# Kernel optimization log

Measured on AMD Instinct MI355X. Metric: run time of the kernel, lower is better.

The kernel has to match this reference:

```python
import jax, jax.numpy as jnp
import numpy as np

B, A, D = 1024, 200, 128
H = 8
DH = D // H
TANH_CLIP = 10.0


def setup_inputs() -> dict:
    key = jax.random.key(0)
    k = jax.random.split(key, 8)
    agent_embd = jax.random.normal(k[0], (B, A, D), dtype=jnp.float32)
    # old_action must be a permutation per row (no revisits under the mask)
    old_action = jax.vmap(lambda kk: jax.random.permutation(kk, A))(
        jax.random.split(k[1], B)).astype(jnp.int32)
    s = 0.02
    W_placeholder = jax.random.uniform(k[2], (D,), jnp.float32, -1.0, 1.0)
    W_node = jax.random.normal(k[3], (D, 3 * D), jnp.float32) * s   # project_node_embeddings
    W_fixed = jax.random.normal(k[4], (D, D), jnp.float32) * s      # project_fixed_context
    W_step = jax.random.normal(k[5], (D, D), jnp.float32) * s       # project_step_context
    W_out = jax.random.normal(k[6], (D, D), jnp.float32) * s        # project_out
    return {"agent_embd": agent_embd, "old_action": old_action,
            "W_placeholder": W_placeholder, "W_node": W_node,
            "W_fixed": W_fixed, "W_step": W_step, "W_out": W_out}


def _decode(agent_embd, old_action, W_placeholder, W_node, W_fixed, W_step, W_out):
    b_, a_, d_ = agent_embd.shape
    inv_sqrt_dh = np.float32(1.0 / np.sqrt(DH))
    inv_sqrt_d = np.float32(1.0 / np.sqrt(d_))
    batch_ix = jnp.arange(b_)

    # _precompute: fixed context + per-head K/V + logit keys
    graph_embed = agent_embd.mean(axis=1)                      # [B, D]
    fixed_ctx = graph_embed @ W_fixed                          # [B, D]
    proj = agent_embd @ W_node                                 # [B, A, 3D]
    gK, gV, logit_K = jnp.split(proj, 3, axis=-1)              # each [B, A, D]
    gK = gK.reshape(b_, a_, H, DH).transpose(2, 0, 1, 3)       # [H, B, A, dh]
    gV = gV.reshape(b_, a_, H, DH).transpose(2, 0, 1, 3)       # [H, B, A, dh]

    def step(carry, xs):
        mask, prev = carry                                     # [B, A] bool, [B] int
        i, act = xs
        gathered = agent_embd[batch_ix, prev]                  # [B, D]
        step_ctx = jnp.where(i == 0, W_placeholder[None, :], gathered)
        query = fixed_ctx + step_ctx @ W_step                  # [B, D]
        mask = jnp.where(i > 0, mask.at[batch_ix, prev].set(True), mask)

        Q = query.reshape(b_, H, DH).transpose(1, 0, 2)        # [H, B, dh]
        compat = jnp.einsum('hbd,hbad->hba', Q, gK) * inv_sqrt_dh
        compat = jnp.where(mask[None, :, :], -jnp.inf, compat)  # mask_inner
        attn = jax.nn.softmax(compat, axis=-1)                 # [H, B, A]
        heads = jnp.einsum('hba,hbad->hbd', attn, gV)          # [H, B, dh]
        glimpse = heads.transpose(1, 0, 2).reshape(b_, d_) @ W_out  # [B, D]

        logits = jnp.einsum('bd,bad->ba', glimpse, logit_K) * inv_sqrt_d
        logits = jnp.tanh(logits) * TANH_CLIP
        logits = jnp.where(mask, -jnp.inf, logits)             # mask_logits
        log_p = jax.nn.log_softmax(logits, axis=-1)            # [B, A]
        lp_sel = log_p[batch_ix, act]                          # [B]
        return (mask, act), lp_sel

    mask0 = jnp.zeros((b_, a_), dtype=bool)
    prev0 = jnp.zeros((b_,), dtype=old_action.dtype)
    xs = (jnp.arange(a_), old_action.T)
    _, lps = jax.lax.scan(step, (mask0, prev0), xs)            # lps: [A, B]
    return old_action, lps.sum(axis=0)


def reference(agent_embd, old_action, W_placeholder, W_node, W_fixed, W_step, W_out):
    return _decode(agent_embd, old_action, W_placeholder, W_node, W_fixed, W_step, W_out)
```

## Files before the change

### kernel.cpp

```cpp
#include <hip/hip_runtime.h>
#include <cstdint>
#include <cstddef>

#define BB 1024
#define AA 200
#define DD 128
#define HH 8
#define N3 384

typedef unsigned short u16;
typedef unsigned int u32;
typedef __attribute__((ext_vector_type(8))) short bf16x8;
typedef __attribute__((ext_vector_type(4))) float f32x4;

__device__ __forceinline__ float bf2f(u16 v){ return __uint_as_float(((u32)v) << 16); }
__device__ __forceinline__ u16 f2bf(float f){
  u32 u = __float_as_uint(f);
  u32 r = u + 0x7fffu + ((u >> 16) & 1u);
  return (u16)(r >> 16);
}
__device__ __forceinline__ u16 f2bf_trunc(float f){
  return (u16)(__float_as_uint(f) >> 16);
}
__device__ __forceinline__ bf16x8 pack8(float4 a, float4 b){
  bf16x8 o;
  o[0] = (short)f2bf(a.x); o[1] = (short)f2bf(a.y);
  o[2] = (short)f2bf(a.z); o[3] = (short)f2bf(a.w);
  o[4] = (short)f2bf(b.x); o[5] = (short)f2bf(b.y);
  o[6] = (short)f2bf(b.z); o[7] = (short)f2bf(b.w);
  return o;
}

__global__ void k_act_rank(const int* __restrict__ oa, float* __restrict__ out0,
                           int* __restrict__ rank){
  int m = blockIdx.x * 256 + threadIdx.x;
  if (m >= BB*AA) return;
  int v = oa[m];
  out0[m] = (float)v;
  int b = m / AA;
  int j = m - b*AA;
  rank[b*AA + v] = j;
}

__global__ void k_prep(const float* __restrict__ Wn, const float* __restrict__ Ws,
                       const float* __restrict__ Wo,
                       u16* __restrict__ WnT, u16* __restrict__ WsT,
                       u16* __restrict__ WoT){
  int idx = blockIdx.x * 256 + threadIdx.x;
  if (idx < 49152){
    int n = idx >> 7, k = idx & 127;
    WnT[idx] = f2bf(Wn[k*N3 + n]);
  } else if (idx < 65536){
    int j = idx - 49152;
    int n = j >> 7, k = j & 127;
    WsT[j] = f2bf(Ws[k*DD + n]);
  } else if (idx < 81920){
    int j = idx - 65536;
    int n = j >> 7, k = j & 127;
    WoT[j] = f2bf(Wo[k*DD + n]);
  }
}

__global__ void k_fixed(const float* __restrict__ E, const float* __restrict__ Wf,
                        float* __restrict__ fixedc){
  int b = blockIdx.x;
  int d = threadIdx.x;
  __shared__ float ge[DD];
  const float* Eb = E + (size_t)b*AA*DD;
  float s = 0.f;
  for (int a = 0; a < AA; ++a) s += Eb[a*DD + d];
  ge[d] = s * (1.0f/AA);
  __syncthreads();
  float acc = 0.f;
  for (int k = 0; k < DD; ++k) acc = fmaf(ge[k], Wf[k*DD + d], acc);
  fixedc[b*DD + d] = acc;
}

__global__ __launch_bounds__(256) void k_proj_mfma(const float* __restrict__ E,
                                                   const u16* __restrict__ WnT,
                                                   u16* __restrict__ proj){
  const int t = threadIdx.x;
  const int w = t >> 6, L = t & 63;
  const int l16 = L & 15, lq = L >> 4;
  const int m0 = blockIdx.x * 128;
  const int n0 = blockIdx.y * 128;
  const int row0 = m0 + w*32;

  f32x4 acc[2][8] = {};
  const float* Arow0 = E + (size_t)(row0 + l16)*DD;
  const float* Arow1 = Arow0 + (size_t)16*DD;
  #pragma unroll
  for (int ks = 0; ks < 4; ++ks){
    int ko = ks*32 + lq*8;
    bf16x8 a0 = pack8(*(const float4*)(Arow0 + ko), *(const float4*)(Arow0 + ko + 4));
    bf16x8 a1 = pack8(*(const float4*)(Arow1 + ko), *(const float4*)(Arow1 + ko + 4));
    #pragma unroll
    for (int nt = 0; nt < 8; ++nt){
      union { uint4 u; bf16x8 v; } bb;
      bb.u = *(const uint4*)(WnT + (size_t)(n0 + nt*16 + l16)*DD + ko);
      acc[0][nt] = __builtin_amdgcn_mfma_f32_16x16x32_bf16(a0, bb.v, acc[0][nt], 0, 0, 0);
      acc[1][nt] = __builtin_amdgcn_mfma_f32_16x16x32_bf16(a1, bb.v, acc[1][nt], 0, 0, 0);
    }
  }
  #pragma unroll
  for (int mt = 0; mt < 2; ++mt)
    #pragma unroll
    for (int r = 0; r < 4; ++r){
      int row = row0 + mt*16 + lq*4 + r;
      u16* dst = proj + (size_t)row*N3 + n0;
      #pragma unroll
      for (int nt = 0; nt < 8; ++nt)
        dst[nt*16 + l16] = f2bf(acc[mt][nt][r]);
    }
}

__global__ __launch_bounds__(256) void k_query_mfma(const float* __restrict__ E,
                                                    const int* __restrict__ oa,
                                                    const float* __restrict__ Wp,
                                                    const u16* __restrict__ WsT,
                                                    const float* __restrict__ fixedc,
                                                    u16* __restrict__ qhg){
  const int t = threadIdx.x;
  const int w = t >> 6, L = t & 63;
  const int l16 = L & 15, lq = L >> 4;
  const int m0 = blockIdx.x * 128;
  const int row0 = m0 + w*32;

  const float* src[2];
  #pragma unroll
  for (int mt = 0; mt < 2; ++mt){
    int q = row0 + mt*16 + l16;
    int b = q / AA, i = q - b*AA;
    src[mt] = (i == 0) ? Wp : (E + (size_t)(b*AA + oa[b*AA + i - 1])*DD);
  }

  f32x4 acc[2][8] = {};
  #pragma unroll
  for (int ks = 0; ks < 4; ++ks){
    int ko = ks*32 + lq*8;
    bf16x8 a0 = pack8(*(const float4*)(src[0] + ko), *(const float4*)(src[0] + ko + 4));
    bf16x8 a1 = pack8(*(const float4*)(src[1] + ko), *(const float4*)(src[1] + ko + 4));
    #pragma unroll
    for (int nt = 0; nt < 8; ++nt){
      union { uint4 u; bf16x8 v; } bb;
      bb.u = *(const uint4*)(WsT + (size_t)(nt*16 + l16)*DD + ko);
      acc[0][nt] = __builtin_amdgcn_mfma_f32_16x16x32_bf16(a0, bb.v, acc[0][nt], 0, 0, 0);
      acc[1][nt] = __builtin_amdgcn_mfma_f32_16x16x32_bf16(a1, bb.v, acc[1][nt], 0, 0, 0);
    }
  }
  #pragma unroll
  for (int mt = 0; mt < 2; ++mt)
    #pragma unroll
    for (int r = 0; r < 4; ++r){
      int row = row0 + mt*16 + lq*4 + r;
      int b = row / AA;
      const float* fc = fixedc + (size_t)b*DD;
      u16* dst = qhg + (size_t)row*DD;
      #pragma unroll
      for (int nt = 0; nt < 8; ++nt)
        dst[nt*16 + l16] = f2bf((acc[mt][nt][r] + fc[nt*16 + l16]) * 0.25f);
    }
}

#define KSTR 24
#define VSTR 232
__global__ __launch_bounds__(256) void k_attn(const u16* __restrict__ proj,
                                              const int* __restrict__ rank,
                                              u16* __restrict__ qhg){
  __shared__ __align__(16) u16 KL[208*KSTR];
  __shared__ __align__(16) u16 VT[16*VSTR];
  __shared__ __align__(16) u16 P [4][16*VSTR];
  const int b = blockIdx.x;
  const int h = blockIdx.y;
  const int t = threadIdx.x;
  const int w = t >> 6, L = t & 63;
  const int l16 = L & 15, lq = L >> 4;

  for (int idx = t; idx < 208*KSTR; idx += 256) KL[idx] = 0;
  for (int idx = t; idx < 16*VSTR; idx += 256) VT[idx] = 0;
  {
    u16* Pw = P[w];
    for (int idx = L; idx < 16*VSTR; idx += 64) Pw[idx] = 0;
  }

  if (t < AA){
    const u16* src = proj + ((size_t)(b*AA + t))*N3 + h*16;
    uint4 k0 = *(const uint4*)(src);
    uint4 k1 = *(const uint4*)(src + 8);
    *(uint4*)&KL[t*KSTR]     = k0;
    *(uint4*)&KL[t*KSTR + 8] = k1;
    const u16* sv = src + 128;
    u16 d16[16];
    *(uint4*)(d16)   = *(const uint4*)(sv);
    *(uint4*)(d16+8) = *(const uint4*)(sv+8);
    #pragma unroll
    for (int d = 0; d < 16; ++d) VT[d*VSTR + t] = d16[d];
  }

  int ra[13];
  #pragma unroll
  for (int at = 0; at < 13; ++at){
    int a = at*16 + l16;
    ra[at] = (a < AA) ? rank[b*AA + a] : -1;
  }
  __syncthreads();

  u16* Qbase = qhg + (size_t)b*AA*DD + h*16;
  u16* Pw = P[w];

  const bf16x8 zf = {0,0,0,0,0,0,0,0};
  for (int it = w; it < 13; it += 4){
    bf16x8 qf = zf;
    int qi = it*16 + l16;
    if (lq < 2 && qi < AA){
      union { uint4 u; bf16x8 v; } tmp;
      tmp.u = *(const uint4*)(Qbase + (size_t)qi*DD + lq*8);
      qf = tmp.v;
    }
    f32x4 S[13];
    #pragma unroll
    for (int at = 0; at < 13; ++at){
      bf16x8 kf = zf;
      if (lq < 2){
        union { uint4 u; bf16x8 v; } tmp;
        tmp.u = *(const uint4*)&KL[(at*16 + l16)*KSTR + lq*8];
        kf = tmp.v;
      }
      f32x4 z = {0.f,0.f,0.f,0.f};
      S[at] = __builtin_amdgcn_mfma_f32_16x16x32_bf16(qf, kf, z, 0, 0, 0);
    }
    #pragma unroll
    for (int at = 0; at < 13; ++at)
      #pragma unroll
      for (int r = 0; r < 4; ++r){
        int i = it*16 + lq*4 + r;
        S[at][r] = (ra[at] < i) ? -__builtin_inff() : S[at][r];
      }
    float inv[4];
    #pragma unroll
    for (int r = 0; r < 4; ++r){
      float m = S[0][r];
      #pragma unroll
      for (int at = 1; at < 13; ++at) m = fmaxf(m, S[at][r]);
      #pragma unroll
      for (int off = 1; off < 16; off <<= 1) m = fmaxf(m, __shfl_xor(m, off));
      float sum = 0.f;
      #pragma unroll
      for (int at = 0; at < 13; ++at){
        float e = __expf(S[at][r] - m);
        S[at][r] = e; sum += e;
      }
      #pragma unroll
      for (int off = 1; off < 16; off <<= 1) sum += __shfl_xor(sum, off);
      inv[r] = 1.0f / sum;
    }
    #pragma unroll
    for (int at = 0; at < 13; ++at)
      #pragma unroll
      for (int r = 0; r < 4; ++r)
        Pw[(lq*4 + r)*VSTR + at*16 + l16] = f2bf_trunc(S[at][r]);
    f32x4 acc = {0.f,0.f,0.f,0.f};
    #pragma unroll
    for (int kb = 0; kb < 7; ++kb){
      union { uint4 u; bf16x8 v; } pa, vb;
      pa.u = *(const uint4*)&Pw[l16*VSTR + kb*32 + lq*8];
      vb.u = *(const uint4*)&VT[l16*VSTR + kb*32 + lq*8];
      acc = __builtin_amdgcn_mfma_f32_16x16x32_bf16(pa.v, vb.v, acc, 0, 0, 0);
    }
    #pragma unroll
    for (int r = 0; r < 4; ++r){
      int i = it*16 + lq*4 + r;
      if (i < AA) Qbase[(size_t)i*DD + l16] = f2bf(acc[r] * inv[r]);
    }
  }
}

__global__ __launch_bounds__(256) void k_glimpse_mfma(const u16* __restrict__ qhg,
                                                      const u16* __restrict__ WoT,
                                                      u16* __restrict__ proj){
  const int t = threadIdx.x;
  const int w = t >> 6, L = t & 63;
  const int l16 = L & 15, lq = L >> 4;
  const int m0 = blockIdx.x * 128;
  const int row0 = m0 + w*32;

  f32x4 acc[2][8] = {};
  const u16* Arow0 = qhg + (size_t)(row0 + l16)*DD;
  const u16* Arow1 = Arow0 + (size_t)16*DD;
  #pragma unroll
  for (int ks = 0; ks < 4; ++ks){
    int ko = ks*32 + lq*8;
    union { uint4 u; bf16x8 v; } a0, a1;
    a0.u = *(const uint4*)(Arow0 + ko);
    a1.u = *(const uint4*)(Arow1 + ko);
    #pragma unroll
    for (int nt = 0; nt < 8; ++nt){
      union { uint4 u; bf16x8 v; } bb;
      bb.u = *(const uint4*)(WoT + (size_t)(nt*16 + l16)*DD + ko);
      acc[0][nt] = __builtin_amdgcn_mfma_f32_16x16x32_bf16(a0.v, bb.v, acc[0][nt], 0, 0, 0);
      acc[1][nt] = __builtin_amdgcn_mfma_f32_16x16x32_bf16(a1.v, bb.v, acc[1][nt], 0, 0, 0);
    }
  }
  #pragma unroll
  for (int mt = 0; mt < 2; ++mt)
    #pragma unroll
    for (int r = 0; r < 4; ++r){
      int row = row0 + mt*16 + lq*4 + r;
      u16* dst = proj + (size_t)row*N3;
      #pragma unroll
      for (int nt = 0; nt < 8; ++nt)
        dst[nt*16 + l16] = f2bf(acc[mt][nt][r]);
    }
}

__global__ __launch_bounds__(256) void k_logits(const u16* __restrict__ proj,
                                                const int* __restrict__ rank,
                                                const int* __restrict__ oa,
                                                float* __restrict__ outlps){
  __shared__ float red[4];
  const int b = blockIdx.x;
  const int t = threadIdx.x;
  const int w = t >> 6, L = t & 63;
  const int l16 = L & 15, lq = L >> 4;
  const float inv_sqrt_d = 0.08838834764831843f;

  const u16* Gbase  = proj + (size_t)b*AA*N3;
  const u16* LKbase = Gbase + 256;

  int ra[13];
  #pragma unroll
  for (int at = 0; at < 13; ++at){
    int a = at*16 + l16;
    ra[at] = (a < AA) ? rank[b*AA + a] : -1;
  }

  float lp_part = 0.f;

  for (int it = w; it < 13; it += 4){
    bf16x8 af[4];
    {
      const u16* arow = Gbase + (size_t)(it*16 + l16)*N3;
      #pragma unroll
      for (int kb = 0; kb < 4; ++kb){
        union { uint4 u; bf16x8 v; } tmp;
        tmp.u = *(const uint4*)(arow + kb*32 + lq*8);
        af[kb] = tmp.v;
      }
    }
    f32x4 S[13];
    #pragma unroll
    for (int at = 0; at < 13; ++at){
      const u16* brow = LKbase + (size_t)(at*16 + l16)*N3;
      f32x4 acc = {0.f,0.f,0.f,0.f};
      #pragma unroll
      for (int kb = 0; kb < 4; ++kb){
        union { uint4 u; bf16x8 v; } tmp;
        tmp.u = *(const uint4*)(brow + kb*32 + lq*8);
        acc = __builtin_amdgcn_mfma_f32_16x16x32_bf16(af[kb], tmp.v, acc, 0, 0, 0);
      }
      S[at] = acc;
    }
    #pragma unroll
    for (int at = 0; at < 13; ++at)
      #pragma unroll
      for (int r = 0; r < 4; ++r){
        int i = it*16 + lq*4 + r;
        float x = S[at][r] * inv_sqrt_d;
        float e = __expf(2.0f*x);
        float th = 1.0f - 2.0f/(e + 1.0f);
        S[at][r] = (ra[at] < i) ? -__builtin_inff() : 10.0f*th;
      }
    #pragma unroll
    for (int r = 0; r < 4; ++r){
      int i = it*16 + lq*4 + r;
      float m = S[0][r];
      #pragma unroll
      for (int at = 1; at < 13; ++at) m = fmaxf(m, S[at][r]);
      #pragma unroll
      for (int off = 1; off < 16; off <<= 1) m = fmaxf(m, __shfl_xor(m, off));
      float sum = 0.f;
      #pragma unroll
      for (int at = 0; at < 13; ++at) sum += __expf(S[at][r] - m);
      #pragma unroll
      for (int off = 1; off < 16; off <<= 1) sum += __shfl_xor(sum, off);
      if (i < AA){
        float lse = m + __logf(sum);
        int act = oa[b*AA + i];
        if ((act & 15) == l16){
          int at0 = act >> 4;
          #pragma unroll
          for (int at = 0; at < 13; ++at)
            if (at == at0) lp_part += S[at][r] - lse;
        }
      }
    }
  }
  #pragma unroll
  for (int off = 1; off < 64; off <<= 1) lp_part += __shfl_xor(lp_part, off);
  if (L == 0) red[w] = lp_part;
  __syncthreads();
  if (t == 0) outlps[b] = red[0] + red[1] + red[2] + red[3];
}

extern "C" void kernel_launch(void* const* d_in, const int* in_sizes, int n_in,
                              void* d_out, int out_size, void* d_ws, size_t ws_size,
                              hipStream_t stream){
  const float* E  = (const float*)d_in[0];
  const int*   oa = (const int*)d_in[1];
  const float* Wp = (const float*)d_in[2];
  const float* Wn = (const float*)d_in[3];
  const float* Wf = (const float*)d_in[4];
  const float* Ws = (const float*)d_in[5];
  const float* Wo = (const float*)d_in[6];
  float* out = (float*)d_out;

  char* ws = (char*)d_ws;
  int*   rank   = (int*)ws;
  float* fixedc = (float*)(ws + 819200);
  u16*   proj   = (u16*)(ws + 1343488);
  u16*   qhg    = (u16*)(ws + 158629888);
  u16*   WnT    = (u16*)(ws + 211058688);
  u16*   WsT    = (u16*)(ws + 211156992);
  u16*   WoT    = (u16*)(ws + 211189760);

  k_act_rank<<<dim3((BB*AA)/256), 256, 0, stream>>>(oa, out, rank);
  k_prep<<<dim3(320), 256, 0, stream>>>(Wn, Ws, Wo, WnT, WsT, WoT);
  k_fixed<<<dim3(BB), 128, 0, stream>>>(E, Wf, fixedc);
  k_proj_mfma<<<dim3((BB*AA)/128, N3/128), 256, 0, stream>>>(E, WnT, proj);
  k_query_mfma<<<dim3((BB*AA)/128), 256, 0, stream>>>(E, oa, Wp, WsT, fixedc, qhg);
  k_attn<<<dim3(BB, HH), 256, 0, stream>>>(proj, rank, qhg);
  k_glimpse_mfma<<<dim3((BB*AA)/128), 256, 0, stream>>>(qhg, WoT, proj);
  k_logits<<<dim3(BB), 256, 0, stream>>>(proj, rank, oa, out + BB*AA);
}
```

Before: 740.3 us.

## Keep attention probabilities in registers via transposed MFMA, drop P shared buffer

The attention kernel computes S transposed (K as the A operand) so that each lane holds a whole column of scores. The probabilities can then be packed into bf16 in registers and fed straight into 16x16x16 MFMAs against V, with no round trip through a per-wave shared-memory P buffer. Ranks are staged in shared memory, only padding regions are zeroed, the softmax reductions need only two cross-lane shuffles, and the grid is reordered so that the heads of one batch run adjacently. Launch bounds now request higher occupancy, which risks register pressure with the S[13] array held in registers.

```diff
diff --git a/kernel.cpp b/kernel.cpp
--- a/kernel.cpp
+++ b/kernel.cpp
@@ -11,16 +11,24 @@
 typedef unsigned short u16;
 typedef unsigned int u32;
 typedef __attribute__((ext_vector_type(8))) short bf16x8;
+typedef __attribute__((ext_vector_type(4))) short bf16x4;
 typedef __attribute__((ext_vector_type(4))) float f32x4;
+
+#if defined(__HIP_DEVICE_COMPILE__)
+  #if __has_builtin(__builtin_amdgcn_mfma_f32_16x16x16_bf16)
+    #define MFMA16(a,b,c) __builtin_amdgcn_mfma_f32_16x16x16_bf16(a,b,c,0,0,0)
+  #else
+    #define MFMA16(a,b,c) __builtin_amdgcn_mfma_f32_16x16x16bf16_1k(a,b,c,0,0,0)
+  #endif
+#else
+  #define MFMA16(a,b,c) (c)
+#endif
 
 __device__ __forceinline__ float bf2f(u16 v){ return __uint_as_float(((u32)v) << 16); }
 __device__ __forceinline__ u16 f2bf(float f){
   u32 u = __float_as_uint(f);
   u32 r = u + 0x7fffu + ((u >> 16) & 1u);
   return (u16)(r >> 16);
-}
-__device__ __forceinline__ u16 f2bf_trunc(float f){
-  return (u16)(__float_as_uint(f) >> 16);
 }
 __device__ __forceinline__ bf16x8 pack8(float4 a, float4 b){
   bf16x8 o;
@@ -164,24 +172,24 @@
 
 #define KSTR 24
 #define VSTR 232
-__global__ __launch_bounds__(256) void k_attn(const u16* __restrict__ proj,
-                                              const int* __restrict__ rank,
-                                              u16* __restrict__ qhg){
+__global__ __launch_bounds__(256, 4) void k_attn(const u16* __restrict__ proj,
+                                                 const int* __restrict__ rank,
+                                                 u16* __restrict__ qhg){
   __shared__ __align__(16) u16 KL[208*KSTR];
   __shared__ __align__(16) u16 VT[16*VSTR];
-  __shared__ __align__(16) u16 P [4][16*VSTR];
-  const int b = blockIdx.x;
-  const int h = blockIdx.y;
+  __shared__ __align__(16) int rankL[208];
+  const int h = blockIdx.x;
+  const int b = blockIdx.y;
   const int t = threadIdx.x;
   const int w = t >> 6, L = t & 63;
   const int l16 = L & 15, lq = L >> 4;
 
-  for (int idx = t; idx < 208*KSTR; idx += 256) KL[idx] = 0;
-  for (int idx = t; idx < 16*VSTR; idx += 256) VT[idx] = 0;
-  {
-    u16* Pw = P[w];
-    for (int idx = L; idx < 16*VSTR; idx += 64) Pw[idx] = 0;
-  }
+  if (t < 192) KL[200*KSTR + t] = 0;
+  for (int idx = t; idx < 16*32; idx += 256){
+    int d = idx >> 5, c = idx & 31;
+    VT[d*VSTR + 200 + c] = 0;
+  }
+  if (t < 208) rankL[t] = (t < AA) ? rank[b*AA + t] : -1;
 
   if (t < AA){
     const u16* src = proj + ((size_t)(b*AA + t))*N3 + h*16;
@@ -196,81 +204,72 @@
     #pragma unroll
     for (int d = 0; d < 16; ++d) VT[d*VSTR + t] = d16[d];
   }
-
-  int ra[13];
-  #pragma unroll
-  for (int at = 0; at < 13; ++at){
-    int a = at*16 + l16;
-    ra[at] = (a < AA) ? rank[b*AA + a] : -1;
-  }
   __syncthreads();
 
-  u16* Qbase = qhg + (size_t)b*AA*DD + h*16;
-  u16* Pw = P[w];
-
-  const bf16x8 zf = {0,0,0,0,0,0,0,0};
+  u16* Qb = qhg + (size_t)b*AA*DD + h*16;
+  const bf16x8 zf8 = {0,0,0,0,0,0,0,0};
+
   for (int it = w; it < 13; it += 4){
-    bf16x8 qf = zf;
-    int qi = it*16 + l16;
-    if (lq < 2 && qi < AA){
+    const int i = it*16 + l16;
+    bf16x8 qf = zf8;
+    if (lq < 2 && i < AA){
       union { uint4 u; bf16x8 v; } tmp;
-      tmp.u = *(const uint4*)(Qbase + (size_t)qi*DD + lq*8);
+      tmp.u = *(const uint4*)(Qb + (size_t)i*DD + lq*8);
       qf = tmp.v;
     }
     f32x4 S[13];
     #pragma unroll
     for (int at = 0; at < 13; ++at){
-      bf16x8 kf = zf;
+      bf16x8 kf = zf8;
       if (lq < 2){
         union { uint4 u; bf16x8 v; } tmp;
         tmp.u = *(const uint4*)&KL[(at*16 + l16)*KSTR + lq*8];
         kf = tmp.v;
       }
       f32x4 z = {0.f,0.f,0.f,0.f};
-      S[at] = __builtin_amdgcn_mfma_f32_16x16x32_bf16(qf, kf, z, 0, 0, 0);
-    }
+      S[at] = __builtin_amdgcn_mfma_f32_16x16x32_bf16(kf, qf, z, 0, 0, 0);
+    }
+    #pragma unroll
+    for (int at = 0; at < 13; ++at){
+      int4 rr = *(const int4*)&rankL[at*16 + lq*4];
+      S[at][0] = (rr.x < i) ? -__builtin_inff() : S[at][0];
+      S[at][1] = (rr.y < i) ? -__builtin_inff() : S[at][1];
+      S[at][2] = (rr.z < i) ? -__builtin_inff() : S[at][2];
+      S[at][3] = (rr.w < i) ? -__builtin_inff() : S[at][3];
+    }
+    float m = S[0][0];
     #pragma unroll
     for (int at = 0; at < 13; ++at)
       #pragma unroll
+      for (int r = 0; r < 4; ++r) m = fmaxf(m, S[at][r]);
+    m = fmaxf(m, __shfl_xor(m, 16));
+    m = fmaxf(m, __shfl_xor(m, 32));
+    float sum = 0.f;
+    #pragma unroll
+    for (int at = 0; at < 13; ++at)
+      #pragma unroll
       for (int r = 0; r < 4; ++r){
-        int i = it*16 + lq*4 + r;
-        S[at][r] = (ra[at] < i) ? -__builtin_inff() : S[at][r];
-      }
-    float inv[4];
-    #pragma unroll
-    for (int r = 0; r < 4; ++r){
-      float m = S[0][r];
-      #pragma unroll
-      for (int at = 1; at < 13; ++at) m = fmaxf(m, S[at][r]);
-      #pragma unroll
-      for (int off = 1; off < 16; off <<= 1) m = fmaxf(m, __shfl_xor(m, off));
-      float sum = 0.f;
-      #pragma unroll
-      for (int at = 0; at < 13; ++at){
         float e = __expf(S[at][r] - m);
         S[at][r] = e; sum += e;
       }
-      #pragma unroll
-      for (int off = 1; off < 16; off <<= 1) sum += __shfl_xor(sum, off);
-      inv[r] = 1.0f / sum;
-    }
-    #pragma unroll
-    for (int at = 0; at < 13; ++at)
-      #pragma unroll
-      for (int r = 0; r < 4; ++r)
-        Pw[(lq*4 + r)*VSTR + at*16 + l16] = f2bf_trunc(S[at][r]);
+    sum += __shfl_xor(sum, 16);
+    sum += __shfl_xor(sum, 32);
+    const float inv = 1.0f / sum;
     f32x4 acc = {0.f,0.f,0.f,0.f};
     #pragma unroll
-    for (int kb = 0; kb < 7; ++kb){
-      union { uint4 u; bf16x8 v; } pa, vb;
-      pa.u = *(const uint4*)&Pw[l16*VSTR + kb*32 + lq*8];
-      vb.u = *(const uint4*)&VT[l16*VSTR + kb*32 + lq*8];
-      acc = __builtin_amdgcn_mfma_f32_16x16x32_bf16(pa.v, vb.v, acc, 0, 0, 0);
-    }
-    #pragma unroll
-    for (int r = 0; r < 4; ++r){
-      int i = it*16 + lq*4 + r;
-      if (i < AA) Qbase[(size_t)i*DD + l16] = f2bf(acc[r] * inv[r]);
+    for (int at = 0; at < 13; ++at){
+      u32 p0 = (__float_as_uint(S[at][0]) >> 16) | (__float_as_uint(S[at][1]) & 0xffff0000u);
+      u32 p1 = (__float_as_uint(S[at][2]) >> 16) | (__float_as_uint(S[at][3]) & 0xffff0000u);
+      union { u32 u[2]; bf16x4 v; } pf; pf.u[0] = p0; pf.u[1] = p1;
+      union { uint2 u; bf16x4 v; } vf;
+      vf.u = *(const uint2*)&VT[l16*VSTR + at*16 + lq*4];
+      acc = MFMA16(vf.v, pf.v, acc);
+    }
+    if (i < AA){
+      uint2 o;
+      o.x = (u32)f2bf(acc[0]*inv) | ((u32)f2bf(acc[1]*inv) << 16);
+      o.y = (u32)f2bf(acc[2]*inv) | ((u32)f2bf(acc[3]*inv) << 16);
+      *(uint2*)(Qb + (size_t)i*DD + lq*4) = o;
     }
   }
 }
@@ -428,7 +427,7 @@
   k_fixed<<<dim3(BB), 128, 0, stream>>>(E, Wf, fixedc);
   k_proj_mfma<<<dim3((BB*AA)/128, N3/128), 256, 0, stream>>>(E, WnT, proj);
   k_query_mfma<<<dim3((BB*AA)/128), 256, 0, stream>>>(E, oa, Wp, WsT, fixedc, qhg);
-  k_attn<<<dim3(BB, HH), 256, 0, stream>>>(proj, rank, qhg);
+  k_attn<<<dim3(HH, BB), 256, 0, stream>>>(proj, rank, qhg);
   k_glimpse_mfma<<<dim3((BB*AA)/128), 256, 0, stream>>>(qhg, WoT, proj);
   k_logits<<<dim3(BB), 256, 0, stream>>>(proj, rank, oa, out + BB*AA);
 }
```

Measured after the change: 836.3 us. 1.13x slower.
